# Optimization experiments

Hardware: AMD Instinct MI355X
Metric: run time of the kernel (lower is better)

The kernel has to match this reference:

```python
import jax, jax.numpy as jnp
import numpy as np

N_NODES = 100000
N_EDGES = 1600000
FEAT = 128
HID = 128
N_EDGE_TYPES = 8


def _glorot(key, shape):
    fan_in, fan_out = shape[0], shape[1]
    lim = jnp.sqrt(6.0 / (fan_in + fan_out)).astype(jnp.float32)
    return jax.random.uniform(key, shape, jnp.float32, -lim, lim)


def setup_inputs() -> dict:
    key = jax.random.key(0)
    ks = jax.random.split(key, 16)
    inp = {
        "x": jax.random.normal(ks[0], (N_NODES, FEAT), jnp.float32),
        "edge_index": jax.random.randint(ks[1], (2, N_EDGES), 0, N_NODES, jnp.int64 if jax.config.jax_enable_x64 else jnp.int32),
        "edge_attr": jax.random.randint(ks[2], (N_EDGES,), 0, N_EDGE_TYPES, jnp.int32),
        # x_encode
        "Wx": _glorot(ks[3], (FEAT, HID)), "bx": jnp.zeros((HID,), jnp.float32),
        # edge-attr embedding table
        "emb": _glorot(ks[4], (N_EDGE_TYPES, HID)),
        # GINEConv eps (train_eps=True, init 0)
        "eps1": jnp.zeros((), jnp.float32), "eps2": jnp.zeros((), jnp.float32),
        # nn1: Linear-ReLU-Linear-ReLU-Linear
        "W1a": _glorot(ks[5], (HID, HID)), "b1a": jnp.zeros((HID,), jnp.float32),
        "W1b": _glorot(ks[6], (HID, HID)), "b1b": jnp.zeros((HID,), jnp.float32),
        "W1c": _glorot(ks[7], (HID, HID)), "b1c": jnp.zeros((HID,), jnp.float32),
        # nn2
        "W2a": _glorot(ks[8], (HID, HID)), "b2a": jnp.zeros((HID,), jnp.float32),
        "W2b": _glorot(ks[9], (HID, HID)), "b2b": jnp.zeros((HID,), jnp.float32),
        "W2c": _glorot(ks[10], (HID, HID)), "b2c": jnp.zeros((HID,), jnp.float32),
    }
    return inp


def _mlp(h, Wa, ba, Wb, bb, Wc, bc):
    h = jax.nn.relu(h @ Wa + ba)
    h = jax.nn.relu(h @ Wb + bb)
    return h @ Wc + bc


def reference(x, edge_index, edge_attr, Wx, bx, emb, eps1, eps2,
              W1a, b1a, W1b, b1b, W1c, b1c,
              W2a, b2a, W2b, b2b, W2c, b2c):
    n = x.shape[0]
    src, dst = edge_index[0], edge_index[1]
    h = jax.nn.relu(x @ Wx + bx)              # [N, HID]
    ea = emb[edge_attr]                       # [E, HID]

    def gine(h, eps, Wa, ba, Wb, bb, Wc, bc):
        msg = jax.nn.relu(h[src] + ea)        # gather + add + relu  [E, HID]
        agg = jax.ops.segment_sum(msg, dst, num_segments=n)  # scatter-add [N, HID]
        return _mlp((1.0 + eps) * h + agg, Wa, ba, Wb, bb, Wc, bc)

    h = jax.nn.relu(gine(h, eps1, W1a, b1a, W1b, b1b, W1c, b1c))
    # dropout is identity in eval-mode reference
    h = jax.nn.relu(gine(h, eps2, W2a, b2a, W2b, b2b, W2c, b2c))
    return h
```

## Files before the change

kernel.cpp:

```cpp
#include <hip/hip_runtime.h>
#include <hip/hip_bf16.h>
#include <cstdint>
#include <cstddef>

#define NN 100000
#define NNP 100096
#define NE 1600000
#define HID 128
#define NBUK 196
#define NBB 391
#define ECH 4096

typedef unsigned int u32;
typedef unsigned short u16;
typedef __bf16 bf16x8 __attribute__((ext_vector_type(8)));
typedef float f32x16 __attribute__((ext_vector_type(16)));

__device__ inline u32 pack2(float a, float b) {
    u16 x = __builtin_bit_cast(u16, (__bf16)a);
    u16 y = __builtin_bit_cast(u16, (__bf16)b);
    return (u32)x | ((u32)y << 16);
}
__device__ inline float b2f(u16 v) { return __uint_as_float((u32)v << 16); }


__global__ __launch_bounds__(256) void bincount_kernel(const int* __restrict__ dst,
                                                       u32* __restrict__ bcnt) {
    __shared__ u32 lh[256];
    int tid = threadIdx.x;
    lh[tid] = 0;
    __syncthreads();
    int e0 = blockIdx.x * ECH;
    for (int i = tid; i < ECH; i += 256) {
        int e = e0 + i;
        if (e < NE) atomicAdd(&lh[(u32)dst[e] >> 9], 1u);
    }
    __syncthreads();
    if (tid < NBUK && lh[tid]) atomicAdd(&bcnt[tid], lh[tid]);
}

__global__ __launch_bounds__(256) void bucketscan_kernel(const u32* __restrict__ bcnt,
                                                         u32* __restrict__ boff,
                                                         u32* __restrict__ bcur) {
    __shared__ u32 s[256];
    int t = threadIdx.x;
    u32 c = (t < NBUK) ? bcnt[t] : 0u;
    s[t] = c;
    __syncthreads();
    for (int off = 1; off < 256; off <<= 1) {
        u32 add = (t >= off) ? s[t - off] : 0u;
        __syncthreads();
        s[t] += add;
        __syncthreads();
    }
    u32 excl = s[t] - c;
    if (t <= NBUK) boff[t] = excl;
    if (t < NBUK) bcur[t] = excl;
}

__global__ __launch_bounds__(256) void binscatter_kernel(const int* __restrict__ src,
                                                         const int* __restrict__ dst,
                                                         const int* __restrict__ attr,
                                                         u32* __restrict__ bcur,
                                                         u32* __restrict__ binned) {
    __shared__ u32 lh[256], rb[256], rc[256];
    int tid = threadIdx.x;
    lh[tid] = 0; rc[tid] = 0;
    __syncthreads();
    int e0 = blockIdx.x * ECH;
    for (int i = tid; i < ECH; i += 256) {
        int e = e0 + i;
        if (e < NE) atomicAdd(&lh[(u32)dst[e] >> 9], 1u);
    }
    __syncthreads();
    if (tid < NBUK && lh[tid]) rb[tid] = atomicAdd(&bcur[tid], lh[tid]);
    __syncthreads();
    for (int i = tid; i < ECH; i += 256) {
        int e = e0 + i;
        if (e < NE) {
            u32 d = (u32)dst[e];
            u32 b = d >> 9;
            u32 pos = rb[b] + atomicAdd(&rc[b], 1u);
            binned[pos] = (d & 511u) | ((u32)src[e] << 9) | ((u32)attr[e] << 26);
        }
    }
}

__global__ __launch_bounds__(256) void bucketcsr_kernel(const u32* __restrict__ boff,
                                                        const u32* __restrict__ binned,
                                                        u32* __restrict__ rs,
                                                        u32* __restrict__ ep) {
    __shared__ u32 hist[512];
    __shared__ u32 s[256];
    int tid = threadIdx.x;
    int buk = blockIdx.x;
    u32 base = boff[buk], cnt = boff[buk + 1] - base;
    int n0 = buk << 9;
    int nloc = (NN - n0 < 512) ? (NN - n0) : 512;
    hist[tid] = 0; hist[tid + 256] = 0;
    __syncthreads();
    for (u32 i = tid; i < cnt; i += 256)
        atomicAdd(&hist[binned[base + i] & 511u], 1u);
    __syncthreads();
    u32 v0 = hist[2 * tid], v1 = hist[2 * tid + 1];
    u32 ls = v0 + v1;
    s[tid] = ls;
    __syncthreads();
    for (int off = 1; off < 256; off <<= 1) {
        u32 add = (tid >= off) ? s[tid - off] : 0u;
        __syncthreads();
        s[tid] += add;
        __syncthreads();
    }
    u32 excl = s[tid] - ls;
    hist[2 * tid] = excl;
    hist[2 * tid + 1] = excl + v0;
    __syncthreads();
    if (tid < nloc) rs[n0 + tid] = base + hist[tid];
    for (int j = tid + 256; j < nloc; j += 256) rs[n0 + j] = base + hist[j];
    if (buk == NBUK - 1 && tid == 0) rs[NN] = base + cnt;
    __syncthreads();
    for (u32 i = tid; i < cnt; i += 256) {
        u32 v = binned[base + i];
        u32 dl = v & 511u;
        u32 pos = atomicAdd(&hist[dl], 1u);
        ep[base + pos] = ((v >> 9) & 0x1FFFFu) | ((v >> 26) << 20);
    }
}


__global__ __launch_bounds__(256) void wt_kernel(const float* __restrict__ W0,
                                                 const float* __restrict__ W1,
                                                 const float* __restrict__ W2,
                                                 const float* __restrict__ W3,
                                                 const float* __restrict__ W4,
                                                 const float* __restrict__ W5,
                                                 const float* __restrict__ W6,
                                                 u32* __restrict__ Wt) {
    __shared__ float s[64][129];
    int m = blockIdx.x >> 1, h = blockIdx.x & 1;
    const float* W = (m == 0) ? W0 : (m == 1) ? W1 : (m == 2) ? W2 : (m == 3) ? W3
                   : (m == 4) ? W4 : (m == 5) ? W5 : W6;
    int tid = threadIdx.x;
#pragma unroll
    for (int it = 0; it < 8; ++it) {
        int u = it * 256 + tid;
        int r = u >> 5, c4 = (u & 31) * 4;
        float4 v = *(const float4*)&W[(size_t)(64 * h + r) * HID + c4];
        s[r][c4] = v.x; s[r][c4 + 1] = v.y; s[r][c4 + 2] = v.z; s[r][c4 + 3] = v.w;
    }
    __syncthreads();
    u32* outm = Wt + (size_t)m * 8192;
#pragma unroll
    for (int it = 0; it < 16; ++it) {
        int u = it * 256 + tid;
        int n = u >> 5, kpl = u & 31;
        u32 v = pack2(s[2 * kpl][n], s[2 * kpl + 1][n]);
        outm[(size_t)n * 64 + 32 * h + kpl] = v;
    }
}


__global__ __launch_bounds__(256) void agg_kernel(const u16* __restrict__ h,
                                                  const u32* __restrict__ rs,
                                                  const u32* __restrict__ ep,
                                                  const float* __restrict__ emb,
                                                  u16* __restrict__ agg) {
    __shared__ float semb[8 * HID];
    int tid = threadIdx.x;
    ((float4*)semb)[tid] = ((const float4*)emb)[tid];
    __syncthreads();
    int wave = tid >> 6, lane = tid & 63;
    int node = blockIdx.x * 4 + wave;
    u32 s0 = rs[node], s1 = rs[node + 1];
    const u32* h32 = (const u32*)h;
    const float2* e2 = (const float2*)semb;
    float ax = 0.f, ay = 0.f;
    u32 j = s0;
    for (; j + 8 <= s1; j += 8) {
        u32 p[8];
#pragma unroll
        for (int t = 0; t < 8; ++t) p[t] = ep[j + t];
        u32 hv[8];
#pragma unroll
        for (int t = 0; t < 8; ++t) hv[t] = h32[(size_t)(p[t] & 0xFFFFFu) * 64 + lane];
        float2 ev[8];
#pragma unroll
        for (int t = 0; t < 8; ++t) ev[t] = e2[(p[t] >> 20) * 64 + lane];
#pragma unroll
        for (int t = 0; t < 8; ++t) {
            ax += fmaxf(__uint_as_float(hv[t] << 16) + ev[t].x, 0.f);
            ay += fmaxf(__uint_as_float(hv[t] & 0xFFFF0000u) + ev[t].y, 0.f);
        }
    }
    if (j + 4 <= s1) {
        u32 p[4];
#pragma unroll
        for (int t = 0; t < 4; ++t) p[t] = ep[j + t];
        u32 hv[4];
#pragma unroll
        for (int t = 0; t < 4; ++t) hv[t] = h32[(size_t)(p[t] & 0xFFFFFu) * 64 + lane];
        float2 ev[4];
#pragma unroll
        for (int t = 0; t < 4; ++t) ev[t] = e2[(p[t] >> 20) * 64 + lane];
#pragma unroll
        for (int t = 0; t < 4; ++t) {
            ax += fmaxf(__uint_as_float(hv[t] << 16) + ev[t].x, 0.f);
            ay += fmaxf(__uint_as_float(hv[t] & 0xFFFF0000u) + ev[t].y, 0.f);
        }
        j += 4;
    }
    for (; j < s1; j++) {
        u32 p = ep[j];
        u32 hv = h32[(size_t)(p & 0xFFFFFu) * 64 + lane];
        float2 ev = e2[(p >> 20) * 64 + lane];
        ax += fmaxf(__uint_as_float(hv << 16) + ev.x, 0.f);
        ay += fmaxf(__uint_as_float(hv & 0xFFFF0000u) + ev.y, 0.f);
    }
    ((u32*)agg)[(size_t)node * 64 + lane] = pack2(ax, ay);
}


__device__ inline void stageWt(char* sW, const uint4* __restrict__ Wt4, int tid) {
#pragma unroll
    for (int it = 0; it < 8; ++it) {
        int u = it * 256 + tid;
        int n = u >> 4, c = u & 15;
        uint4 v = Wt4[(size_t)n * 16 + c];
        *(uint4*)(sW + n * 256 + ((c * 16) ^ ((n & 15) << 4))) = v;
    }
}

template <int NL, int MODE, bool OUTB>
__global__ __launch_bounds__(256, 2) void mlp_mfma(
    const void* __restrict__ inp, const u16* __restrict__ aggb,
    const float* __restrict__ epsp, void* __restrict__ outp,
    const u32* __restrict__ Wt0, const float* __restrict__ b0,
    const u32* __restrict__ Wt1, const float* __restrict__ b1,
    const u32* __restrict__ Wt2, const float* __restrict__ b2) {
    __shared__ __align__(16) char sA[128 * 256];
    __shared__ __align__(16) char sW[128 * 256];
    int tid = threadIdx.x;
    int row0 = blockIdx.x * 128;

    if (MODE == 0) {
        const float* x = (const float*)inp;
#pragma unroll
        for (int it = 0; it < 16; ++it) {
            int idx = it * 256 + tid;
            int r = idx >> 5, c4 = (idx & 31) * 4;
            int grow = row0 + r;
            uint2 pk = make_uint2(0u, 0u);
            if (grow < NN) {
                float4 v = *(const float4*)&x[(size_t)grow * HID + c4];
                pk.x = pack2(v.x, v.y);
                pk.y = pack2(v.z, v.w);
            }
            *(uint2*)(sA + r * 256 + ((c4 * 2) ^ ((r & 15) << 4))) = pk;
        }
    } else {
        const u16* hin = (const u16*)inp;
        float eps = 1.0f + epsp[0];
#pragma unroll
        for (int it = 0; it < 16; ++it) {
            int idx = it * 256 + tid;
            int r = idx >> 5, c4 = (idx & 31) * 4;
            int grow = row0 + r;
            uint2 pk = make_uint2(0u, 0u);
            if (grow < NN) {
                ushort4 hv = *(const ushort4*)&hin[(size_t)grow * HID + c4];
                ushort4 gv = *(const ushort4*)&aggb[(size_t)grow * HID + c4];
                pk.x = pack2(eps * b2f(hv.x) + b2f(gv.x), eps * b2f(hv.y) + b2f(gv.y));
                pk.y = pack2(eps * b2f(hv.z) + b2f(gv.z), eps * b2f(hv.w) + b2f(gv.w));
            }
            *(uint2*)(sA + r * 256 + ((c4 * 2) ^ ((r & 15) << 4))) = pk;
        }
    }
    stageWt(sW, (const uint4*)Wt0, tid);
    __syncthreads();

    int lane = tid & 63, w = tid >> 6;
    int lo5 = lane & 31, hi = lane >> 5;
    int swzkey = (lo5 & 15) << 4;

#pragma unroll 1
    for (int l = 0; l < NL; ++l) {
        const float* bl = (l == 0) ? b0 : ((l == 1) ? b1 : b2);
        f32x16 acc[4];
#pragma unroll
        for (int nf = 0; nf < 4; ++nf) {
            float bv = bl[nf * 32 + lo5];
#pragma unroll
            for (int i = 0; i < 16; ++i) acc[nf][i] = bv;
        }
#pragma unroll
        for (int kc = 0; kc < 8; ++kc) {
            int koff = kc * 32 + hi * 16;
            bf16x8 a = *(const bf16x8*)(sA + (32 * w + lo5) * 256 + (koff ^ swzkey));
#pragma unroll
            for (int nf = 0; nf < 4; ++nf) {
                bf16x8 bb = *(const bf16x8*)(sW + (nf * 32 + lo5) * 256 + (koff ^ swzkey));
                acc[nf] = __builtin_amdgcn_mfma_f32_32x32x16_bf16(a, bb, acc[nf], 0, 0, 0);
            }
        }
        if (l + 1 < NL) {
            __syncthreads();
            stageWt(sW, (const uint4*)((l == 0) ? Wt1 : Wt2), tid);
#pragma unroll
            for (int nf = 0; nf < 4; ++nf) {
#pragma unroll
                for (int reg = 0; reg < 16; ++reg) {
                    int r32 = (reg & 3) + 8 * (reg >> 2) + 4 * hi;
                    int col = nf * 32 + lo5;
                    float v = fmaxf(acc[nf][reg], 0.f);
                    *(u16*)(sA + (32 * w + r32) * 256 + ((col * 2) ^ ((r32 & 15) << 4))) =
                        __builtin_bit_cast(u16, (__bf16)v);
                }
            }
            __syncthreads();
        } else {
#pragma unroll
            for (int nf = 0; nf < 4; ++nf) {
#pragma unroll
                for (int reg = 0; reg < 16; ++reg) {
                    int r32 = (reg & 3) + 8 * (reg >> 2) + 4 * hi;
                    int grow = row0 + 32 * w + r32;
                    int col = nf * 32 + lo5;
                    float v = fmaxf(acc[nf][reg], 0.f);
                    if (grow < NN) {
                        if (OUTB)
                            ((u16*)outp)[(size_t)grow * HID + col] =
                                __builtin_bit_cast(u16, (__bf16)v);
                        else
                            ((float*)outp)[(size_t)grow * HID + col] = v;
                    }
                }
            }
        }
    }
}


extern "C" void kernel_launch(void* const* d_in, const int* in_sizes, int n_in,
                              void* d_out, int out_size, void* d_ws, size_t ws_size,
                              hipStream_t stream) {
    const float* x    = (const float*)d_in[0];
    const int*   ei   = (const int*)d_in[1];
    const int*   ea   = (const int*)d_in[2];
    const float* Wx   = (const float*)d_in[3];
    const float* bx   = (const float*)d_in[4];
    const float* emb  = (const float*)d_in[5];
    const float* eps1 = (const float*)d_in[6];
    const float* eps2 = (const float*)d_in[7];
    const float* W1a = (const float*)d_in[8],  *b1a = (const float*)d_in[9];
    const float* W1b = (const float*)d_in[10], *b1b = (const float*)d_in[11];
    const float* W1c = (const float*)d_in[12], *b1c = (const float*)d_in[13];
    const float* W2a = (const float*)d_in[14], *b2a = (const float*)d_in[15];
    const float* W2b = (const float*)d_in[16], *b2b = (const float*)d_in[17];
    const float* W2c = (const float*)d_in[18], *b2c = (const float*)d_in[19];
    float* out = (float*)d_out;

    const int* srcp = ei;
    const int* dstp = ei + NE;

    char* ws = (char*)d_ws;
    u16* h16   = (u16*)ws;
    size_t off = (size_t)NNP * HID * 2;
    u16* agg16 = (u16*)(ws + off); off += (size_t)NNP * HID * 2;
    u32* binned = (u32*)agg16;
    u32* rs   = (u32*)(ws + off); off += 400032;
    u32* bcnt = (u32*)(ws + off); off += 256 * 4;
    u32* boff = (u32*)(ws + off); off += 256 * 4;
    u32* bcur = (u32*)(ws + off); off += 256 * 4;
    u32* ep   = (u32*)(ws + off); off += (size_t)NE * 4;
    u32* Wt   = (u32*)(ws + off); off += 7 * 8192 * 4;

    hipMemsetAsync(bcnt, 0, 256 * 4, stream);

    wt_kernel<<<14, 256, 0, stream>>>(Wx, W1a, W1b, W1c, W2a, W2b, W2c, Wt);

    mlp_mfma<1, 0, true><<<NNP / 128, 256, 0, stream>>>(
        x, nullptr, nullptr, h16, Wt, bx, nullptr, nullptr, nullptr, nullptr);

    bincount_kernel<<<NBB, 256, 0, stream>>>(dstp, bcnt);
    bucketscan_kernel<<<1, 256, 0, stream>>>(bcnt, boff, bcur);
    binscatter_kernel<<<NBB, 256, 0, stream>>>(srcp, dstp, ea, bcur, binned);
    bucketcsr_kernel<<<NBUK, 256, 0, stream>>>(boff, binned, rs, ep);

    agg_kernel<<<NN / 4, 256, 0, stream>>>(h16, rs, ep, emb, agg16);
    mlp_mfma<3, 1, true><<<NNP / 128, 256, 0, stream>>>(
        h16, agg16, eps1, h16, Wt + 8192, b1a, Wt + 2 * 8192, b1b, Wt + 3 * 8192, b1c);

    agg_kernel<<<NN / 4, 256, 0, stream>>>(h16, rs, ep, emb, agg16);
    mlp_mfma<3, 1, false><<<NNP / 128, 256, 0, stream>>>(
        h16, agg16, eps2, out, Wt + 4 * 8192, b2a, Wt + 5 * 8192, b2b, Wt + 6 * 8192, b2c);
}
```

Measured before the change: 448.1 us.

## Fuse per-bucket CSR construction into aggregation kernel with LDS edge lists

```diff
diff --git a/kernel.cpp b/kernel.cpp
--- a/kernel.cpp
+++ b/kernel.cpp
@@ -7,9 +7,11 @@
 #define NNP 100096
 #define NE 1600000
 #define HID 128
-#define NBUK 196
+#define BKN 128
+#define NBUK 782
 #define NBB 391
 #define ECH 4096
+#define CAP 2816
 
 typedef unsigned int u32;
 typedef unsigned short u16;
@@ -26,36 +28,48 @@
 
 __global__ __launch_bounds__(256) void bincount_kernel(const int* __restrict__ dst,
                                                        u32* __restrict__ bcnt) {
-    __shared__ u32 lh[256];
+    __shared__ u32 lh[NBUK];
     int tid = threadIdx.x;
-    lh[tid] = 0;
+    for (int i = tid; i < NBUK; i += 256) lh[i] = 0;
     __syncthreads();
     int e0 = blockIdx.x * ECH;
     for (int i = tid; i < ECH; i += 256) {
         int e = e0 + i;
-        if (e < NE) atomicAdd(&lh[(u32)dst[e] >> 9], 1u);
-    }
-    __syncthreads();
-    if (tid < NBUK && lh[tid]) atomicAdd(&bcnt[tid], lh[tid]);
+        if (e < NE) atomicAdd(&lh[(u32)dst[e] >> 7], 1u);
+    }
+    __syncthreads();
+    for (int i = tid; i < NBUK; i += 256)
+        if (lh[i]) atomicAdd(&bcnt[i], lh[i]);
 }
 
 __global__ __launch_bounds__(256) void bucketscan_kernel(const u32* __restrict__ bcnt,
                                                          u32* __restrict__ boff,
                                                          u32* __restrict__ bcur) {
     __shared__ u32 s[256];
+    __shared__ u32 carry;
     int t = threadIdx.x;
-    u32 c = (t < NBUK) ? bcnt[t] : 0u;
-    s[t] = c;
-    __syncthreads();
-    for (int off = 1; off < 256; off <<= 1) {
-        u32 add = (t >= off) ? s[t - off] : 0u;
+    if (t == 0) carry = 0;
+    __syncthreads();
+#pragma unroll 1
+    for (int c = 0; c < 4; ++c) {
+        int idx = c * 256 + t;
+        u32 v = (idx < NBUK) ? bcnt[idx] : 0u;
+        s[t] = v;
         __syncthreads();
-        s[t] += add;
+        for (int off = 1; off < 256; off <<= 1) {
+            u32 a = (t >= off) ? s[t - off] : 0u;
+            __syncthreads();
+            s[t] += a;
+            __syncthreads();
+        }
+        u32 run = carry;
+        u32 excl = run + s[t] - v;
+        if (idx <= NBUK) boff[idx] = excl;
+        if (idx < NBUK) bcur[idx] = excl;
         __syncthreads();
-    }
-    u32 excl = s[t] - c;
-    if (t <= NBUK) boff[t] = excl;
-    if (t < NBUK) bcur[t] = excl;
+        if (t == 255) carry = run + s[255];
+        __syncthreads();
+    }
 }
 
 __global__ __launch_bounds__(256) void binscatter_kernel(const int* __restrict__ src,
@@ -63,68 +77,128 @@
                                                          const int* __restrict__ attr,
                                                          u32* __restrict__ bcur,
                                                          u32* __restrict__ binned) {
-    __shared__ u32 lh[256], rb[256], rc[256];
+    __shared__ u32 lh[NBUK], rb[NBUK], rc[NBUK];
     int tid = threadIdx.x;
-    lh[tid] = 0; rc[tid] = 0;
+    for (int i = tid; i < NBUK; i += 256) { lh[i] = 0; rc[i] = 0; }
     __syncthreads();
     int e0 = blockIdx.x * ECH;
     for (int i = tid; i < ECH; i += 256) {
         int e = e0 + i;
-        if (e < NE) atomicAdd(&lh[(u32)dst[e] >> 9], 1u);
-    }
-    __syncthreads();
-    if (tid < NBUK && lh[tid]) rb[tid] = atomicAdd(&bcur[tid], lh[tid]);
+        if (e < NE) atomicAdd(&lh[(u32)dst[e] >> 7], 1u);
+    }
+    __syncthreads();
+    for (int i = tid; i < NBUK; i += 256)
+        if (lh[i]) rb[i] = atomicAdd(&bcur[i], lh[i]);
     __syncthreads();
     for (int i = tid; i < ECH; i += 256) {
         int e = e0 + i;
         if (e < NE) {
             u32 d = (u32)dst[e];
-            u32 b = d >> 9;
+            u32 b = d >> 7;
             u32 pos = rb[b] + atomicAdd(&rc[b], 1u);
-            binned[pos] = (d & 511u) | ((u32)src[e] << 9) | ((u32)attr[e] << 26);
-        }
-    }
-}
-
-__global__ __launch_bounds__(256) void bucketcsr_kernel(const u32* __restrict__ boff,
-                                                        const u32* __restrict__ binned,
-                                                        u32* __restrict__ rs,
-                                                        u32* __restrict__ ep) {
-    __shared__ u32 hist[512];
+            binned[pos] = (d & 127u) | ((u32)src[e] << 7) | ((u32)attr[e] << 24);
+        }
+    }
+}
+
+
+__global__ __launch_bounds__(256) void bucket_agg_kernel(const u32* __restrict__ boff,
+                                                         const u32* __restrict__ binned,
+                                                         const u16* __restrict__ h,
+                                                         const float* __restrict__ emb,
+                                                         u16* __restrict__ agg) {
+    __shared__ u32 epl[CAP];
+    __shared__ u32 hist[BKN + 1];
+    __shared__ u32 hcur[BKN];
     __shared__ u32 s[256];
+    __shared__ float semb[8 * HID];
     int tid = threadIdx.x;
     int buk = blockIdx.x;
-    u32 base = boff[buk], cnt = boff[buk + 1] - base;
-    int n0 = buk << 9;
-    int nloc = (NN - n0 < 512) ? (NN - n0) : 512;
-    hist[tid] = 0; hist[tid + 256] = 0;
-    __syncthreads();
+    u32 base = boff[buk];
+    u32 cnt = boff[buk + 1] - base;
+
+    if (tid < BKN) hist[tid] = 0;
+    ((float4*)semb)[tid] = ((const float4*)emb)[tid];
+    __syncthreads();
+
     for (u32 i = tid; i < cnt; i += 256)
-        atomicAdd(&hist[binned[base + i] & 511u], 1u);
-    __syncthreads();
-    u32 v0 = hist[2 * tid], v1 = hist[2 * tid + 1];
-    u32 ls = v0 + v1;
-    s[tid] = ls;
+        atomicAdd(&hist[binned[base + i] & 127u], 1u);
+    __syncthreads();
+
+    u32 v = (tid < BKN) ? hist[tid] : 0u;
+    s[tid] = v;
     __syncthreads();
     for (int off = 1; off < 256; off <<= 1) {
-        u32 add = (tid >= off) ? s[tid - off] : 0u;
+        u32 a = (tid >= off) ? s[tid - off] : 0u;
         __syncthreads();
-        s[tid] += add;
+        s[tid] += a;
         __syncthreads();
     }
-    u32 excl = s[tid] - ls;
-    hist[2 * tid] = excl;
-    hist[2 * tid + 1] = excl + v0;
-    __syncthreads();
-    if (tid < nloc) rs[n0 + tid] = base + hist[tid];
-    for (int j = tid + 256; j < nloc; j += 256) rs[n0 + j] = base + hist[j];
-    if (buk == NBUK - 1 && tid == 0) rs[NN] = base + cnt;
-    __syncthreads();
+    if (tid < BKN) {
+        u32 excl = s[tid] - v;
+        hist[tid] = excl;
+        hcur[tid] = excl;
+    }
+    if (tid == 0) hist[BKN] = cnt;
+    __syncthreads();
+
     for (u32 i = tid; i < cnt; i += 256) {
-        u32 v = binned[base + i];
-        u32 dl = v & 511u;
-        u32 pos = atomicAdd(&hist[dl], 1u);
-        ep[base + pos] = ((v >> 9) & 0x1FFFFu) | ((v >> 26) << 20);
+        u32 w = binned[base + i];
+        u32 pos = atomicAdd(&hcur[w & 127u], 1u);
+        epl[pos] = w >> 7;
+    }
+    __syncthreads();
+
+    int wv = tid >> 6, l = tid & 63;
+    const u32* h32 = (const u32*)h;
+    const float2* e2 = (const float2*)semb;
+    int n0 = buk * BKN;
+    for (int n = wv; n < BKN; n += 4) {
+        int gnode = n0 + n;
+        if (gnode >= NN) break;
+        u32 j = hist[n], j1 = hist[n + 1];
+        float ax = 0.f, ay = 0.f;
+        for (; j + 8 <= j1; j += 8) {
+            u32 e[8];
+#pragma unroll
+            for (int t = 0; t < 8; ++t) e[t] = epl[j + t];
+            u32 hv[8];
+#pragma unroll
+            for (int t = 0; t < 8; ++t) hv[t] = h32[(size_t)(e[t] & 0x1FFFFu) * 64 + l];
+            float2 ev[8];
+#pragma unroll
+            for (int t = 0; t < 8; ++t) ev[t] = e2[(e[t] >> 17) * 64 + l];
+#pragma unroll
+            for (int t = 0; t < 8; ++t) {
+                ax += fmaxf(__uint_as_float(hv[t] << 16) + ev[t].x, 0.f);
+                ay += fmaxf(__uint_as_float(hv[t] & 0xFFFF0000u) + ev[t].y, 0.f);
+            }
+        }
+        if (j + 4 <= j1) {
+            u32 e[4];
+#pragma unroll
+            for (int t = 0; t < 4; ++t) e[t] = epl[j + t];
+            u32 hv[4];
+#pragma unroll
+            for (int t = 0; t < 4; ++t) hv[t] = h32[(size_t)(e[t] & 0x1FFFFu) * 64 + l];
+            float2 ev[4];
+#pragma unroll
+            for (int t = 0; t < 4; ++t) ev[t] = e2[(e[t] >> 17) * 64 + l];
+#pragma unroll
+            for (int t = 0; t < 4; ++t) {
+                ax += fmaxf(__uint_as_float(hv[t] << 16) + ev[t].x, 0.f);
+                ay += fmaxf(__uint_as_float(hv[t] & 0xFFFF0000u) + ev[t].y, 0.f);
+            }
+            j += 4;
+        }
+        for (; j < j1; j++) {
+            u32 e = epl[j];
+            u32 hv = h32[(size_t)(e & 0x1FFFFu) * 64 + l];
+            float2 ev = e2[(e >> 17) * 64 + l];
+            ax += fmaxf(__uint_as_float(hv << 16) + ev.x, 0.f);
+            ay += fmaxf(__uint_as_float(hv & 0xFFFF0000u) + ev.y, 0.f);
+        }
+        ((u32*)agg)[(size_t)gnode * 64 + l] = pack2(ax, ay);
     }
 }
 
@@ -158,66 +232,6 @@
         u32 v = pack2(s[2 * kpl][n], s[2 * kpl + 1][n]);
         outm[(size_t)n * 64 + 32 * h + kpl] = v;
     }
-}
-
-
-__global__ __launch_bounds__(256) void agg_kernel(const u16* __restrict__ h,
-                                                  const u32* __restrict__ rs,
-                                                  const u32* __restrict__ ep,
-                                                  const float* __restrict__ emb,
-                                                  u16* __restrict__ agg) {
-    __shared__ float semb[8 * HID];
-    int tid = threadIdx.x;
-    ((float4*)semb)[tid] = ((const float4*)emb)[tid];
-    __syncthreads();
-    int wave = tid >> 6, lane = tid & 63;
-    int node = blockIdx.x * 4 + wave;
-    u32 s0 = rs[node], s1 = rs[node + 1];
-    const u32* h32 = (const u32*)h;
-    const float2* e2 = (const float2*)semb;
-    float ax = 0.f, ay = 0.f;
-    u32 j = s0;
-    for (; j + 8 <= s1; j += 8) {
-        u32 p[8];
-#pragma unroll
-        for (int t = 0; t < 8; ++t) p[t] = ep[j + t];
-        u32 hv[8];
-#pragma unroll
-        for (int t = 0; t < 8; ++t) hv[t] = h32[(size_t)(p[t] & 0xFFFFFu) * 64 + lane];
-        float2 ev[8];
-#pragma unroll
-        for (int t = 0; t < 8; ++t) ev[t] = e2[(p[t] >> 20) * 64 + lane];
-#pragma unroll
-        for (int t = 0; t < 8; ++t) {
-            ax += fmaxf(__uint_as_float(hv[t] << 16) + ev[t].x, 0.f);
-            ay += fmaxf(__uint_as_float(hv[t] & 0xFFFF0000u) + ev[t].y, 0.f);
-        }
-    }
-    if (j + 4 <= s1) {
-        u32 p[4];
-#pragma unroll
-        for (int t = 0; t < 4; ++t) p[t] = ep[j + t];
-        u32 hv[4];
-#pragma unroll
-        for (int t = 0; t < 4; ++t) hv[t] = h32[(size_t)(p[t] & 0xFFFFFu) * 64 + lane];
-        float2 ev[4];
-#pragma unroll
-        for (int t = 0; t < 4; ++t) ev[t] = e2[(p[t] >> 20) * 64 + lane];
-#pragma unroll
-        for (int t = 0; t < 4; ++t) {
-            ax += fmaxf(__uint_as_float(hv[t] << 16) + ev[t].x, 0.f);
-            ay += fmaxf(__uint_as_float(hv[t] & 0xFFFF0000u) + ev[t].y, 0.f);
-        }
-        j += 4;
-    }
-    for (; j < s1; j++) {
-        u32 p = ep[j];
-        u32 hv = h32[(size_t)(p & 0xFFFFFu) * 64 + lane];
-        float2 ev = e2[(p >> 20) * 64 + lane];
-        ax += fmaxf(__uint_as_float(hv << 16) + ev.x, 0.f);
-        ay += fmaxf(__uint_as_float(hv & 0xFFFF0000u) + ev.y, 0.f);
-    }
-    ((u32*)agg)[(size_t)node * 64 + lane] = pack2(ax, ay);
 }
 
 
@@ -367,15 +381,13 @@
     u16* h16   = (u16*)ws;
     size_t off = (size_t)NNP * HID * 2;
     u16* agg16 = (u16*)(ws + off); off += (size_t)NNP * HID * 2;
-    u32* binned = (u32*)agg16;
-    u32* rs   = (u32*)(ws + off); off += 400032;
-    u32* bcnt = (u32*)(ws + off); off += 256 * 4;
-    u32* boff = (u32*)(ws + off); off += 256 * 4;
-    u32* bcur = (u32*)(ws + off); off += 256 * 4;
-    u32* ep   = (u32*)(ws + off); off += (size_t)NE * 4;
+    u32* bcnt = (u32*)(ws + off); off += 800 * 4;
+    u32* boff = (u32*)(ws + off); off += 800 * 4;
+    u32* bcur = (u32*)(ws + off); off += 800 * 4;
+    u32* binned = (u32*)(ws + off); off += (size_t)NE * 4;
     u32* Wt   = (u32*)(ws + off); off += 7 * 8192 * 4;
 
-    hipMemsetAsync(bcnt, 0, 256 * 4, stream);
+    hipMemsetAsync(bcnt, 0, 800 * 4, stream);
 
     wt_kernel<<<14, 256, 0, stream>>>(Wx, W1a, W1b, W1c, W2a, W2b, W2c, Wt);
 
@@ -385,13 +397,12 @@
     bincount_kernel<<<NBB, 256, 0, stream>>>(dstp, bcnt);
     bucketscan_kernel<<<1, 256, 0, stream>>>(bcnt, boff, bcur);
     binscatter_kernel<<<NBB, 256, 0, stream>>>(srcp, dstp, ea, bcur, binned);
-    bucketcsr_kernel<<<NBUK, 256, 0, stream>>>(boff, binned, rs, ep);
-
-    agg_kernel<<<NN / 4, 256, 0, stream>>>(h16, rs, ep, emb, agg16);
+
+    bucket_agg_kernel<<<NBUK, 256, 0, stream>>>(boff, binned, h16, emb, agg16);
     mlp_mfma<3, 1, true><<<NNP / 128, 256, 0, stream>>>(
         h16, agg16, eps1, h16, Wt + 8192, b1a, Wt + 2 * 8192, b1b, Wt + 3 * 8192, b1c);
 
-    agg_kernel<<<NN / 4, 256, 0, stream>>>(h16, rs, ep, emb, agg16);
+    bucket_agg_kernel<<<NBUK, 256, 0, stream>>>(boff, binned, h16, emb, agg16);
     mlp_mfma<3, 1, false><<<NNP / 128, 256, 0, stream>>>(
         h16, agg16, eps2, out, Wt + 4 * 8192, b2a, Wt + 5 * 8192, b2b, Wt + 6 * 8192, b2c);
 }
```

After: 460.8 us. 1.03x slower.
